# Performance work log

Hardware: AMD Instinct MI355X
Metric: run time of the kernel (lower is better)

Reference implementation:

```python
import jax, jax.numpy as jnp
import numpy as np

ETA = 0.1      # self.eta
BETA = 0.05    # self.beta
MU = 0.05      # self.mu
MINI = 1e-6    # mini_val
SEEDS_PER_TOPIC = 10


def setup_inputs() -> dict:
    key = jax.random.key(0)
    k1, k2, k3, k4 = jax.random.split(key, 4)
    B, V, K = 64, 10000, 64
    # sparse-ish bag-of-words counts in {0,1,2}
    batch_BOW = jax.random.randint(k1, (B, V), 0, 3).astype(jnp.float32)
    # disjoint seed words: SEEDS_PER_TOPIC seed words per topic
    seeds = jnp.zeros((V, K), jnp.float32)
    rows = jnp.arange(SEEDS_PER_TOPIC * K)
    cols = jnp.repeat(jnp.arange(K), SEEDS_PER_TOPIC)
    seeds = seeds.at[rows, cols].set(1.0)
    exp_m = jax.random.uniform(k2, (B, K), jnp.float32) * 10.0     # E[m_dk] for docs in batch
    exp_s = jax.random.uniform(k3, (V, K), jnp.float32) * 5.0 * seeds  # E[s_wk], nonzero only at seed entries
    exp_n = jax.random.uniform(k4, (V, K), jnp.float32) * 5.0      # E[n_wk]
    pi = jnp.full((K,), 0.7, jnp.float32)
    return {"batch_BOW": batch_BOW, "seeds": seeds, "exp_m": exp_m,
            "exp_s": exp_s, "exp_n": exp_n, "pi": pi}


def reference(batch_BOW, seeds, exp_m, exp_s, exp_n, pi):
    # Vectorized SCVB0_guided over the whole minibatch (no per-doc Python loop).
    V, K = seeds.shape
    S = seeds.sum(0)                      # [K] number of seed words per topic
    beta_sum = BETA * V                   # self.beta_sum[guided_m]
    mu_sum = MU * S                       # [K]
    exp_s_sum = exp_s.sum(0)              # [K]
    exp_n_sum = exp_n.sum(0)              # [K]

    mask = (batch_BOW > 0).astype(batch_BOW.dtype)[:, :, None]   # [B,V,1] BOW_nonzero gather
    theta = exp_m[:, None, :] + ETA                               # [B,1,K]
    phi_s = (MU + exp_s) / (mu_sum + exp_s_sum)                   # [V,K]
    phi_n = (BETA + exp_n) / (beta_sum + exp_n_sum)               # [V,K]

    g_ss = mask * seeds[None] * theta * phi_s[None] * pi          # [B,V,K]
    g_sr = mask * seeds[None] * theta * phi_n[None] * (1.0 - pi)
    g_rr = mask * (1.0 - seeds[None]) * theta * phi_n[None]

    s_sum = g_ss.sum(-1, keepdims=True) + g_sr.sum(-1, keepdims=True)
    r_sum = g_rr.sum(-1, keepdims=True)
    g_ss = g_ss / (s_sum + MINI)
    g_sr = g_sr / (s_sum + MINI)
    g_rr = g_rr / (r_sum + MINI)

    # seed word <=> word is seed of at least one topic; else use g_rr only
    is_seed = (seeds.sum(1) > 0)[None, :, None]                   # [1,V,1]
    gamma = jnp.where(is_seed, pi * g_ss + (1.0 - pi) * (g_sr + g_rr), g_rr)

    counts = batch_BOW[:, :, None]                                # [B,V,1]
    temp_exp_m_batch = (gamma * counts).sum(1)                    # [B,K]
    temp_exp_n = ((g_sr + g_rr) * counts).sum(0)                  # [V,K] scatter-accumulate
    temp_exp_s = (g_ss * counts).sum(0)                           # [V,K]
    gamma_sr_sum = g_sr.sum((0, 1))                               # [K]
    exp_q_z = (gamma * jnp.log(gamma + MINI)).sum()               # scalar entropy term
    return temp_exp_m_batch, temp_exp_n, temp_exp_s, gamma_sr_sum, exp_q_z
```

## Files before the change

kernel.cpp:

```cpp
#include <hip/hip_runtime.h>
#include <hip/hip_bf16.h>

#define ETA_C  0.1f
#define BETA_C 0.05f
#define MU_C   0.05f
#define MINI_C 1e-6f

typedef __attribute__((ext_vector_type(8))) short short8;
typedef __attribute__((ext_vector_type(4))) float f32x4;

template<int CTRL, int ROWMASK>
__device__ __forceinline__ float dpp_add(float x) {
  int v = __builtin_amdgcn_update_dpp(0, __float_as_int(x), CTRL, ROWMASK, 0xf, true);
  return x + __int_as_float(v);
}

__device__ __forceinline__ float wave_sum(float x) {
  x = dpp_add<0xB1,  0xF>(x);
  x = dpp_add<0x4E,  0xF>(x);
  x = dpp_add<0x141, 0xF>(x);
  x = dpp_add<0x140, 0xF>(x);
  x = dpp_add<0x142, 0xA>(x);
  x = dpp_add<0x143, 0xC>(x);
  return __int_as_float(__builtin_amdgcn_readlane(__float_as_int(x), 63));
}

__device__ __forceinline__ float rl(float x, int k) {
  return __int_as_float(__builtin_amdgcn_readlane(__float_as_int(x), k));
}

__device__ __forceinline__ short bf16r(float x) {
  unsigned u = __float_as_uint(x);
  u += 0x7fffu + ((u >> 16) & 1u);
  return (short)(u >> 16);
}

__device__ __forceinline__ float bf2f(short s) {
  return __uint_as_float(((unsigned)(unsigned short)s) << 16);
}

__global__ __launch_bounds__(256) void sums_kernel(
    const float* __restrict__ seeds, const float* __restrict__ es,
    const float* __restrict__ en, float* __restrict__ part,
    float* __restrict__ out, int V, int rows_per_block, int gsr_off) {
  __shared__ float sh[192];
  int t = threadIdx.x, bx = blockIdx.x;
  if (bx < 16) out[(bx << 8) + t] = 0.f;
  else if (bx == 16 && t < 65) out[gsr_off + t] = 0.f;
  if (t < 192) sh[t] = 0.f;
  __syncthreads();
  int k = t & 63, w = t >> 6;
  int v0 = bx * rows_per_block;
  int v1 = min(v0 + rows_per_block, V);
  float s0 = 0.f, s1 = 0.f, s2 = 0.f;
  for (int v = v0 + w; v < v1; v += 4) {
    int idx = (v << 6) + k;
    s0 += seeds[idx]; s1 += es[idx]; s2 += en[idx];
  }
  atomicAdd(&sh[k], s0);
  atomicAdd(&sh[64 + k], s1);
  atomicAdd(&sh[128 + k], s2);
  __syncthreads();
  if (t < 192) part[t * 256 + bx] = sh[t];
}

__global__ __launch_bounds__(1024, 4) void main_kernel(
    const float* __restrict__ bow,
    const float* __restrict__ seeds,
    const float* __restrict__ exp_m,
    const float* __restrict__ exp_s,
    const float* __restrict__ exp_n,
    const float* __restrict__ pi,
    const float* __restrict__ part,
    float* __restrict__ out,
    int V, int gsr_off, int NB) {
  __shared__ short THbf[4096];
  __shared__ short THTbf[4096];
  __shared__ short TLbf[4096];
  __shared__ short ARRT[1024];
  __shared__ short ASVT[1024];
  __shared__ short ARLT[1024];
  __shared__ short WSRT[2048];
  __shared__ short PKA[2048];
  __shared__ short CIRT[1024];
  __shared__ float RSL[64 * 17];
  __shared__ float SSL[64 * 17];
  __shared__ float L0a[64 * 17];
  __shared__ float L0b[64 * 17];
  __shared__ float sums_sh[192];
  float* NNL = RSL;
  float* red_gsr = SSL;
  float* redq = L0a;

  int t = threadIdx.x;
  int lane = t & 63, w = t >> 6;

  int gd = (int)gridDim.x;
  float sd[3], esv[3], env[3], bwv[3];
  int nt = 0;
#pragma unroll
  for (int i = 0; i < 3; i++) {
    int tile = (int)blockIdx.x + i * gd;
    if (tile < NB) {
      nt = i + 1;
      int v = (tile << 4) + w;
      if (v < V) {
        int rbase = (v << 6) + lane;
        sd[i]  = seeds[rbase];
        esv[i] = exp_s[rbase];
        env[i] = exp_n[rbase];
        bwv[i] = bow[lane * V + v];
      } else {
        sd[i] = 0.f; esv[i] = 0.f; env[i] = 0.f; bwv[i] = 0.f;
      }
    }
  }
  float pik = pi[lane];
  float omp = 1.0f - pik;

#pragma unroll
  for (int i = 0; i < 4; i++) {
    int idx = t + (i << 10);
    int b = idx >> 6, k = idx & 63;
    float th = exp_m[idx] + ETA_C;
    float lth = __logf(th);
    THbf[idx] = bf16r(th);
    THTbf[(k << 6) + b] = bf16r(th);
    TLbf[idx] = bf16r(th * lth);
  }
  if (t < 192) sums_sh[t] = 0.f;
  __syncthreads();
  if (t < 768) {
    int col = t % 192;
    int seg = t / 192;
    const f32x4* p = (const f32x4*)&part[col * 256 + (seg << 6)];
    float s = 0.f;
#pragma unroll
    for (int j = 0; j < 16; j++) {
      f32x4 v4 = p[j];
      s += (v4[0] + v4[1]) + (v4[2] + v4[3]);
    }
    atomicAdd(&sums_sh[col], s);
  }
  __syncthreads();

  int q = lane >> 4, c = lane & 15;
  float acc_g_tot = 0.f, acc_q_tot = 0.f;
  f32x4 accP = {0.f, 0.f, 0.f, 0.f};

#pragma unroll
  for (int it = 0; it < 3; it++) {
    if (it >= nt) break;
    int tile = (int)blockIdx.x + it * gd;
    int v = (tile << 4) + w;
    bool active = (v < V);

    float a_ss = 0.f, a_sr = 0.f, a_rr = 0.f;
    float bowpre = bwv[it];
    bool seedRow = false;
    if (active) {
      float seed = sd[it];
      float es = esv[it];
      float en = env[it];
      float inv_ds = __builtin_amdgcn_rcpf(MU_C * sums_sh[lane] + sums_sh[64 + lane]);
      float inv_dn = __builtin_amdgcn_rcpf(BETA_C * (float)V + sums_sh[128 + lane]);
      float phi_s = (MU_C + es) * inv_ds;
      float phi_n = (BETA_C + en) * inv_dn;
      a_ss = seed * phi_s * pik;
      a_sr = seed * phi_n * omp;
      a_rr = (1.0f - seed) * phi_n;
      seedRow = (__ballot(seed > 0.f) != 0ull);
      float wsv = fmaf(pik, a_ss, omp * a_sr);
      float wrv = seedRow ? omp * a_rr : a_rr;
      float arrl = (a_rr > 0.f) ? a_rr * __logf(a_rr) : 0.f;
      ARRT[(w << 6) + lane] = bf16r(a_rr);
      ASVT[(w << 6) + lane] = bf16r(a_ss + a_sr);
      ARLT[(w << 6) + lane] = bf16r(arrl);
      WSRT[(lane << 5) + w] = bf16r(wsv);
      WSRT[(lane << 5) + 16 + w] = bf16r(wrv);
    } else {
      ARRT[(w << 6) + lane] = 0;
      ASVT[(w << 6) + lane] = 0;
      ARLT[(w << 6) + lane] = 0;
      WSRT[(lane << 5) + w] = 0;
      WSRT[(lane << 5) + 16 + w] = 0;
    }
    __syncthreads();

    {
      int job = w >> 2, mt = w & 3;
      const short* Amat = (job == 3) ? TLbf : THbf;
      const short* Bmat = (job == 0) ? ARRT : (job == 1) ? ASVT
                         : (job == 2) ? ARLT : ARRT;
      float* Cd = (job == 0) ? RSL : (job == 1) ? SSL : (job == 2) ? L0a : L0b;
      f32x4 acc = {0.f, 0.f, 0.f, 0.f};
      int arow = (mt << 4) + c;
#pragma unroll
      for (int s = 0; s < 2; s++) {
        short8 af = *(const short8*)&Amat[(arow << 6) + (s << 5) + (q << 3)];
        short8 bf = *(const short8*)&Bmat[(c << 6) + (s << 5) + (q << 3)];
        acc = __builtin_amdgcn_mfma_f32_16x16x32_bf16(af, bf, acc, 0, 0, 0);
      }
#pragma unroll
      for (int r = 0; r < 4; r++)
        Cd[((mt << 4) + (q << 2) + r) * 17 + c] = acc[r];
    }
    __syncthreads();

    float acc_s = 0.f, acc_g = 0.f, acc_qk = 0.f, acc_qb = 0.f;
    if (active) {
      float rsv = RSL[lane * 17 + w];
      float ssv = SSL[lane * 17 + w];
      float ivx = __builtin_amdgcn_rcpf(ssv + MINI_C);
      float ivy = __builtin_amdgcn_rcpf(rsv + MINI_C);
      float cis = bowpre * ivx;
      float cirr = bowpre * ivy;
      PKA[(lane << 5) + w] = bf16r(cis);
      PKA[(lane << 5) + 16 + w] = bf16r(cirr);
      CIRT[(w << 6) + lane] = bf16r(cirr);
      if (!seedRow) {
        float Lb = L0a[lane * 17 + w] + L0b[lane * 17 + w];
        float q0 = (bowpre > 0.f) ? ivy : 0.f;
        float q1 = q0 * __logf(ivy);
        acc_qb = fmaf(q0, Lb, q1 * rsv);
        out[4096 + V * 64 + (v << 6) + lane] = 0.f;
      } else {
        float acc_n = 0.f;
        unsigned long long m = __ballot(bowpre > 0.f);
        while (m) {
          int b = __builtin_amdgcn_readfirstlane(__builtin_ctzll(m));
          m &= (m - 1);
          float cb = rl(bowpre, b);
          float is = rl(ivx, b), ir = rl(ivy, b);
          float th = bf2f(THbf[(b << 6) + lane]);
          float gss = th * a_ss * is;
          float gsr = th * a_sr * is;
          float grr = th * a_rr * ir;
          float gnr = gsr + grr;
          float gamma = fmaf(pik, gss, omp * gnr);
          acc_n = fmaf(gnr, cb, acc_n);
          acc_s = fmaf(gss, cb, acc_s);
          acc_g += gsr;
          acc_qk = fmaf(gamma, __logf(gamma + MINI_C), acc_qk);
        }
        out[4096 + (v << 6) + lane] = acc_n;
        out[4096 + V * 64 + (v << 6) + lane] = acc_s;
      }
    } else {
      PKA[(lane << 5) + w] = 0;
      PKA[(lane << 5) + 16 + w] = 0;
      CIRT[(w << 6) + lane] = 0;
    }
    acc_g_tot += acc_g;
    acc_q_tot += acc_qk + acc_qb;
    __syncthreads();

    {
      int tm = w >> 2, tn = w & 3;
      short8 af = *(const short8*)&PKA[(((tm << 4) + c) << 5) + (q << 3)];
      short8 bf = *(const short8*)&WSRT[(((tn << 4) + c) << 5) + (q << 3)];
      accP = __builtin_amdgcn_mfma_f32_16x16x32_bf16(af, bf, accP, 0, 0, 0);
      if (w >= 12) {
        int mt = w - 12;
        f32x4 an = {0.f, 0.f, 0.f, 0.f};
#pragma unroll
        for (int s = 0; s < 2; s++) {
          short8 a2 = *(const short8*)&THTbf[(((mt << 4) + c) << 6) + (s << 5) + (q << 3)];
          short8 b2 = *(const short8*)&CIRT[(c << 6) + (s << 5) + (q << 3)];
          an = __builtin_amdgcn_mfma_f32_16x16x32_bf16(a2, b2, an, 0, 0, 0);
        }
#pragma unroll
        for (int r = 0; r < 4; r++)
          NNL[((mt << 4) + (q << 2) + r) * 17 + c] = an[r];
      }
    }
    __syncthreads();

    if (active && !seedRow)
      out[4096 + (v << 6) + lane] = a_rr * NNL[lane * 17 + w];
  }

  {
    int tm = w >> 2, tn = w & 3;
#pragma unroll
    for (int r = 0; r < 4; r++) {
      int brow = (tm << 4) + (q << 2) + r;
      int kcol = (tn << 4) + c;
      float val = accP[r] * bf2f(THbf[(brow << 6) + kcol]);
      atomicAdd(&out[(brow << 6) + kcol], val);
    }
  }
  __syncthreads();
  red_gsr[t] = acc_g_tot;
  float qzw = wave_sum(acc_q_tot);
  if (lane == 0) redq[w] = qzw;
  __syncthreads();

  if (w == 0) {
    float g = 0.f;
#pragma unroll
    for (int j = 0; j < 16; j++) g += red_gsr[(j << 6) + lane];
    if (g != 0.f) atomicAdd(&out[gsr_off + lane], g);
    if (t == 0) {
      float qs = 0.f;
#pragma unroll
      for (int j = 0; j < 16; j++) qs += redq[j];
      atomicAdd(&out[gsr_off + 64], qs);
    }
  }
}

extern "C" void kernel_launch(void* const* d_in, const int* in_sizes, int n_in,
                              void* d_out, int out_size, void* d_ws,
                              size_t ws_size, hipStream_t stream) {
  (void)n_in; (void)out_size; (void)ws_size;
  const float* bow   = (const float*)d_in[0];
  const float* seeds = (const float*)d_in[1];
  const float* exp_m = (const float*)d_in[2];
  const float* exp_s = (const float*)d_in[3];
  const float* exp_n = (const float*)d_in[4];
  const float* pi    = (const float*)d_in[5];
  int K = in_sizes[5];
  int V = in_sizes[1] / K;
  float* out = (float*)d_out;
  float* part = (float*)d_ws;

  int NB = (V + 15) / 16;
  int NP = NB < 256 ? NB : 256;
  int gsr_off = 4096 + 2 * V * 64;
  int rpb = (V + 255) / 256;

  sums_kernel<<<256, 256, 0, stream>>>(seeds, exp_s, exp_n, part, out, V, rpb,
                                       gsr_off);
  main_kernel<<<NP, 1024, 0, stream>>>(bow, seeds, exp_m, exp_s, exp_n, pi,
                                       part, out, V, gsr_off, NB);
}
```

Before: 105.2 us.

## Fuse column-sum prepass into main kernel via cooperative grid sync

Measured after the change: 213.7 us. 2.03x slower.

```diff
diff --git a/kernel.cpp b/kernel.cpp
--- a/kernel.cpp
+++ b/kernel.cpp
@@ -1,5 +1,8 @@
 #include <hip/hip_runtime.h>
 #include <hip/hip_bf16.h>
+#include <hip/hip_cooperative_groups.h>
+
+namespace cg = cooperative_groups;
 
 #define ETA_C  0.1f
 #define BETA_C 0.05f
@@ -39,41 +42,16 @@
   return __uint_as_float(((unsigned)(unsigned short)s) << 16);
 }
 
-__global__ __launch_bounds__(256) void sums_kernel(
-    const float* __restrict__ seeds, const float* __restrict__ es,
-    const float* __restrict__ en, float* __restrict__ part,
-    float* __restrict__ out, int V, int rows_per_block, int gsr_off) {
-  __shared__ float sh[192];
-  int t = threadIdx.x, bx = blockIdx.x;
-  if (bx < 16) out[(bx << 8) + t] = 0.f;
-  else if (bx == 16 && t < 65) out[gsr_off + t] = 0.f;
-  if (t < 192) sh[t] = 0.f;
-  __syncthreads();
-  int k = t & 63, w = t >> 6;
-  int v0 = bx * rows_per_block;
-  int v1 = min(v0 + rows_per_block, V);
-  float s0 = 0.f, s1 = 0.f, s2 = 0.f;
-  for (int v = v0 + w; v < v1; v += 4) {
-    int idx = (v << 6) + k;
-    s0 += seeds[idx]; s1 += es[idx]; s2 += en[idx];
-  }
-  atomicAdd(&sh[k], s0);
-  atomicAdd(&sh[64 + k], s1);
-  atomicAdd(&sh[128 + k], s2);
-  __syncthreads();
-  if (t < 192) part[t * 256 + bx] = sh[t];
-}
-
-__global__ __launch_bounds__(1024, 4) void main_kernel(
+__global__ __launch_bounds__(1024, 4) void fused_kernel(
     const float* __restrict__ bow,
     const float* __restrict__ seeds,
     const float* __restrict__ exp_m,
     const float* __restrict__ exp_s,
     const float* __restrict__ exp_n,
     const float* __restrict__ pi,
-    const float* __restrict__ part,
+    float* __restrict__ part,
     float* __restrict__ out,
-    int V, int gsr_off, int NB) {
+    int V, int gsr_off, int NB, int rpb) {
   __shared__ short THbf[4096];
   __shared__ short THTbf[4096];
   __shared__ short TLbf[4096];
@@ -94,13 +72,13 @@
 
   int t = threadIdx.x;
   int lane = t & 63, w = t >> 6;
-
-  int gd = (int)gridDim.x;
+  int bx = (int)blockIdx.x, gd = (int)gridDim.x;
+
   float sd[3], esv[3], env[3], bwv[3];
   int nt = 0;
 #pragma unroll
   for (int i = 0; i < 3; i++) {
-    int tile = (int)blockIdx.x + i * gd;
+    int tile = bx + i * gd;
     if (tile < NB) {
       nt = i + 1;
       int v = (tile << 4) + w;
@@ -118,6 +96,12 @@
   float pik = pi[lane];
   float omp = 1.0f - pik;
 
+  if (bx < 16) {
+    if (t < 256) out[(bx << 8) + t] = 0.f;
+  } else if (bx == 16 && t < 65) {
+    out[gsr_off + t] = 0.f;
+  }
+
 #pragma unroll
   for (int i = 0; i < 4; i++) {
     int idx = t + (i << 10);
@@ -130,6 +114,26 @@
   }
   if (t < 192) sums_sh[t] = 0.f;
   __syncthreads();
+
+  {
+    int v0 = bx * rpb, v1 = min(v0 + rpb, V);
+    float s0 = 0.f, s1 = 0.f, s2 = 0.f;
+    for (int v = v0 + w; v < v1; v += 16) {
+      int idx = (v << 6) + lane;
+      s0 += seeds[idx]; s1 += exp_s[idx]; s2 += exp_n[idx];
+    }
+    atomicAdd(&sums_sh[lane], s0);
+    atomicAdd(&sums_sh[64 + lane], s1);
+    atomicAdd(&sums_sh[128 + lane], s2);
+  }
+  __syncthreads();
+  if (t < 192) part[t * 256 + bx] = sums_sh[t];
+
+  __threadfence();
+  cg::this_grid().sync();
+
+  if (t < 192) sums_sh[t] = 0.f;
+  __syncthreads();
   if (t < 768) {
     int col = t % 192;
     int seg = t / 192;
@@ -151,7 +155,7 @@
 #pragma unroll
   for (int it = 0; it < 3; it++) {
     if (it >= nt) break;
-    int tile = (int)blockIdx.x + it * gd;
+    int tile = bx + it * gd;
     int v = (tile << 4) + w;
     bool active = (v < V);
 
@@ -326,12 +330,12 @@
   float* part = (float*)d_ws;
 
   int NB = (V + 15) / 16;
-  int NP = NB < 256 ? NB : 256;
   int gsr_off = 4096 + 2 * V * 64;
   int rpb = (V + 255) / 256;
 
-  sums_kernel<<<256, 256, 0, stream>>>(seeds, exp_s, exp_n, part, out, V, rpb,
-                                       gsr_off);
-  main_kernel<<<NP, 1024, 0, stream>>>(bow, seeds, exp_m, exp_s, exp_n, pi,
-                                       part, out, V, gsr_off, NB);
-}
+  void* args[] = {(void*)&bow, (void*)&seeds, (void*)&exp_m, (void*)&exp_s,
+                  (void*)&exp_n, (void*)&pi, (void*)&part, (void*)&out,
+                  (void*)&V, (void*)&gsr_off, (void*)&NB, (void*)&rpb};
+  hipLaunchCooperativeKernel((void*)fused_kernel, dim3(256), dim3(1024),
+                             args, 0, stream);
+}
```
